# Kernel tuning notes

Measured on AMD Instinct MI355X. Metric: run time of the kernel, lower is better.

Reference implementation:

```python
import jax, jax.numpy as jnp
import numpy as np

T, B, D = 2048, 1, 1024
N_HEAD, D_HEAD, D_FF = 16, 64, 4096
LN_EPS = 1e-5


def layer_norm(x, g, b):
    m = jnp.mean(x, axis=-1, keepdims=True)
    v = jnp.mean(jnp.square(x - m), axis=-1, keepdims=True)
    return (x - m) * jax.lax.rsqrt(v + LN_EPS) * g + b


def rel_shift(x):
    # x: (qlen, klen, bsz, n_head) -> Transformer-XL relative shift
    q, k, b, h = x.shape
    zp = jnp.zeros((q, 1, b, h), dtype=x.dtype)
    x = jnp.concatenate([zp, x], axis=1)            # (q, k+1, b, h)
    x = x.reshape(k + 1, q, b, h)[1:].reshape(q, k, b, h)
    return x


def setup_inputs() -> dict:
    key = jax.random.key(0)
    ks = jax.random.split(key, 12)
    s = lambda fan: 1.0 / np.sqrt(fan)
    inp = {
        "input": jax.random.normal(ks[0], (T, B, D), jnp.float32),
        "pos": jax.random.normal(ks[1], (T, 1, D), jnp.float32),
        "r_w_bias": jax.random.normal(ks[2], (N_HEAD, D_HEAD), jnp.float32) * 0.02,
        "r_r_bias": jax.random.normal(ks[3], (N_HEAD, D_HEAD), jnp.float32) * 0.02,
        # causal mask: True = masked (future positions)
        "mask": jnp.triu(jnp.ones((T, T), dtype=bool), k=1),
        "ln1_g": jnp.ones((D,), jnp.float32),
        "ln1_b": jnp.zeros((D,), jnp.float32),
        "qkv_w": jax.random.normal(ks[4], (D, 3 * D), jnp.float32) * s(D),
        "r_w": jax.random.normal(ks[5], (D, D), jnp.float32) * s(D),
        "o_w": jax.random.normal(ks[6], (D, D), jnp.float32) * s(D),
        "ln2_g": jnp.ones((D,), jnp.float32),
        "ln2_b": jnp.zeros((D,), jnp.float32),
        "ff_w1": jax.random.normal(ks[7], (D, D_FF), jnp.float32) * s(D),
        "ff_b1": jnp.zeros((D_FF,), jnp.float32),
        "ff_w2": jax.random.normal(ks[8], (D_FF, D), jnp.float32) * s(D_FF),
        "ff_b2": jnp.zeros((D,), jnp.float32),
    }
    return inp


def reference(input, pos, r_w_bias, r_r_bias, mask, ln1_g, ln1_b, qkv_w, r_w,
              o_w, ln2_g, ln2_b, ff_w1, ff_b1, ff_w2, ff_b2):
    scale = 1.0 / np.sqrt(D_HEAD)
    # preprocess_attn: layernorm
    q_in = layer_norm(input, ln1_g, ln1_b)                      # (T,B,D)
    w_heads = jnp.einsum('tbd,de->tbe', q_in, qkv_w)            # (T,B,3D)
    w_q, w_k, w_v = jnp.split(w_heads, 3, axis=-1)
    w_q = w_q.reshape(T, B, N_HEAD, D_HEAD)
    w_k = w_k.reshape(T, B, N_HEAD, D_HEAD)
    w_v = w_v.reshape(T, B, N_HEAD, D_HEAD)
    r_k = (pos[:, 0] @ r_w).reshape(T, N_HEAD, D_HEAD)          # (T,h,dh)

    AC = jnp.einsum('ibnd,jbnd->ijbn', w_q + r_w_bias, w_k)     # (T,T,B,h)
    BD = rel_shift(jnp.einsum('ibnd,jnd->ijbn', w_q + r_r_bias, r_k))
    score = (AC + BD) * scale
    score = jnp.where(mask[:, :, None, None], jnp.finfo(score.dtype).min, score)
    probs = jax.nn.softmax(score, axis=1)                       # coverage
    attn_vec = jnp.einsum('ijbn,jbnd->ibnd', probs, w_v).reshape(T, B, D)
    attn_out = jnp.einsum('tbd,de->tbe', attn_vec, o_w)
    # postprocess_attn: (dropout=identity) + residual
    x = input + attn_out
    # FFN block: layernorm > linear-relu-linear > residual
    y = layer_norm(x, ln2_g, ln2_b)
    y = jax.nn.relu(jnp.einsum('tbd,df->tbf', y, ff_w1) + ff_b1)
    y = jnp.einsum('tbf,fd->tbd', y, ff_w2) + ff_b2
    x = x + y
    return x, probs
```

## Files before the change

### kernel.cpp

```cpp
#include <hip/hip_runtime.h>
#include <hip/hip_bf16.h>
#include <stdint.h>

using bf16 = __hip_bfloat16;
using short8 = __attribute__((ext_vector_type(8))) short;
using f32x4 = __attribute__((ext_vector_type(4))) float;

#define T_SEQ 2048
#define DMODEL 1024
#define NHEAD 16
#define DHEAD 64
#define DFF 4096

struct __align__(8) bf16x4 { bf16 x, y, z, w; };

__device__ __forceinline__ void async_cp16(const bf16* g, bf16* l) {
  __builtin_amdgcn_global_load_lds(
      (const __attribute__((address_space(1))) uint32_t*)g,
      (__attribute__((address_space(3))) uint32_t*)l, 16, 0, 0);
}

__global__ __launch_bounds__(256) void transpose_all(
    const float* __restrict__ s0, bf16* __restrict__ d0,
    const float* __restrict__ s1, bf16* __restrict__ d1,
    const float* __restrict__ s2, bf16* __restrict__ d2,
    const float* __restrict__ s3, bf16* __restrict__ d3,
    const float* __restrict__ s4, bf16* __restrict__ d4,
    const float* __restrict__ s5, bf16* __restrict__ d5) {
  __shared__ float tile[32][33];
  int b = blockIdx.x;
  int tx = threadIdx.x, ty = threadIdx.y;
  if (b >= 13312) {
    int idx = (b - 13312) * 256 + ty * 32 + tx;
    float4 v = ((const float4*)s5)[idx];
    bf16x4 o{__float2bfloat16(v.x), __float2bfloat16(v.y),
             __float2bfloat16(v.z), __float2bfloat16(v.w)};
    ((bf16x4*)d5)[idx] = o;
    return;
  }
  const float* src; bf16* dst; int R, C, t;
  if (b < 3072)      { src = s0; dst = d0; R = 1024; C = 3072; t = b; }
  else if (b < 4096) { src = s1; dst = d1; R = 1024; C = 1024; t = b - 3072; }
  else if (b < 5120) { src = s2; dst = d2; R = 1024; C = 1024; t = b - 4096; }
  else if (b < 9216) { src = s3; dst = d3; R = 1024; C = 4096; t = b - 5120; }
  else               { src = s4; dst = d4; R = 4096; C = 1024; t = b - 9216; }
  int tcols = C >> 5;
  int bx = (t % tcols) * 32;
  int by = (t / tcols) * 32;
#pragma unroll
  for (int r = 0; r < 32; r += 8)
    tile[ty + r][tx] = src[(long)(by + ty + r) * C + bx + tx];
  __syncthreads();
#pragma unroll
  for (int r = 0; r < 32; r += 8)
    dst[(long)(bx + ty + r) * R + by + tx] = __float2bfloat16(tile[tx][ty + r]);
}

__global__ __launch_bounds__(256) void ln_cvt(const float* __restrict__ x,
                                              const float* __restrict__ g,
                                              const float* __restrict__ b,
                                              bf16* __restrict__ out) {
  int row = blockIdx.x;
  int tid = threadIdx.x;
  float4 v = ((const float4*)(x + (long)row * DMODEL))[tid];
  float s = v.x + v.y + v.z + v.w;
  float s2 = v.x * v.x + v.y * v.y + v.z * v.z + v.w * v.w;
#pragma unroll
  for (int off = 32; off > 0; off >>= 1) {
    s += __shfl_down(s, off);
    s2 += __shfl_down(s2, off);
  }
  __shared__ float ss[4], ss2[4];
  int wave = tid >> 6, lane = tid & 63;
  if (lane == 0) { ss[wave] = s; ss2[wave] = s2; }
  __syncthreads();
  s = ss[0] + ss[1] + ss[2] + ss[3];
  s2 = ss2[0] + ss2[1] + ss2[2] + ss2[3];
  float mean = s * (1.0f / DMODEL);
  float var = s2 * (1.0f / DMODEL) - mean * mean;
  float rstd = rsqrtf(var + 1e-5f);
  float4 gg = ((const float4*)g)[tid];
  float4 bb = ((const float4*)b)[tid];
  bf16x4 o{__float2bfloat16((v.x - mean) * rstd * gg.x + bb.x),
           __float2bfloat16((v.y - mean) * rstd * gg.y + bb.y),
           __float2bfloat16((v.z - mean) * rstd * gg.z + bb.z),
           __float2bfloat16((v.w - mean) * rstd * gg.w + bb.w)};
  ((bf16x4*)(out + (long)row * DMODEL))[tid] = o;
}

__global__ __launch_bounds__(256) void ff2_init(const float* __restrict__ xws,
                                                const float* __restrict__ b2,
                                                float* __restrict__ out) {
  int idx = blockIdx.x * 256 + threadIdx.x;
  float4 x = ((const float4*)xws)[idx];
  float4 b = ((const float4*)b2)[idx & 255];
  float4 o{x.x + b.x, x.y + b.y, x.z + b.z, x.w + b.w};
  ((float4*)out)[idx] = o;
}

template <int BM, int BN, class Epi>
__global__ __launch_bounds__(256) void gemm_bt(const bf16* __restrict__ A,
                                               const bf16* __restrict__ Bt,
                                               int M, int N, int K,
                                               long aZstride, long bZstride, Epi epi) {
  constexpr int BK = 32;
  constexpr int MT = BM / 32;
  constexpr int NT = BN / 32;
  __shared__ bf16 As[BM * BK];
  __shared__ bf16 Bs[BN * BK];

  const int bm = blockIdx.y, bn = blockIdx.x, z = blockIdx.z;
  const bf16* Ab = A + (long)z * aZstride;
  const bf16* Bb = Bt + (long)z * bZstride;

  const int tid = threadIdx.x;
  const int lane = tid & 63;
  const int wave = tid >> 6;
  const int wr = wave >> 1;
  const int wc = wave & 1;
  const int kBeg = epi.kmin(bm, bn, z);
  const int kEnd = epi.kmax(bm, bn, z, K);

  const f32x4 zero4 = {0.f, 0.f, 0.f, 0.f};
  f32x4 acc[MT][NT];
#pragma unroll
  for (int mt = 0; mt < MT; ++mt)
#pragma unroll
    for (int nt = 0; nt < NT; ++nt) acc[mt][nt] = zero4;

  const int sr = tid >> 2;
  const int sc = (tid & 3) * 8;
  const bf16* aG0 = Ab + (long)(bm * BM + sr) * K + kBeg + sc;
  const bf16* aG1 = Ab + (long)(bm * BM + 64 + sr) * K + kBeg + sc;
  bf16* aL0 = As + tid * 8;
  bf16* aL1 = As + 2048 + tid * 8;
  const bf16* bG0 = Bb + (long)(bn * BN + sr) * K + kBeg + sc;
  bf16* bL0 = Bs + tid * 8;
  const bf16* bG1 = Bb + (long)(bn * BN + 64 + sr) * K + kBeg + sc;
  bf16* bL1 = Bs + 2048 + tid * 8;

  const int aRow = wr * (BM / 2) + (lane & 15);
  const int bRow = wc * (BN / 2) + (lane & 15);
  const int kq = (lane >> 4) * 8;

  for (int k0 = kBeg; k0 < kEnd; k0 += BK) {
    __syncthreads();
    async_cp16(aG0, aL0);
    if constexpr (BM == 128) async_cp16(aG1, aL1);
    async_cp16(bG0, bL0);
    if constexpr (BN == 128) async_cp16(bG1, bL1);
    aG0 += BK; bG0 += BK;
    if constexpr (BM == 128) aG1 += BK;
    if constexpr (BN == 128) bG1 += BK;
    __syncthreads();
    short8 af[MT], bfr[NT];
#pragma unroll
    for (int mt = 0; mt < MT; ++mt)
      af[mt] = *(const short8*)(As + (aRow + mt * 16) * BK + kq);
#pragma unroll
    for (int nt = 0; nt < NT; ++nt)
      bfr[nt] = *(const short8*)(Bs + (bRow + nt * 16) * BK + kq);
#pragma unroll
    for (int mt = 0; mt < MT; ++mt)
#pragma unroll
      for (int nt = 0; nt < NT; ++nt)
        acc[mt][nt] = __builtin_amdgcn_mfma_f32_16x16x32_bf16(af[mt], bfr[nt],
                                                              acc[mt][nt], 0, 0, 0);
  }

  const int rBase = (lane >> 4) * 4;
  const int cOff = lane & 15;
#pragma unroll
  for (int mt = 0; mt < MT; ++mt) {
#pragma unroll
    for (int nt = 0; nt < NT; ++nt) {
      int row = bm * BM + wr * (BM / 2) + mt * 16 + rBase;
      int col = bn * BN + wc * (BN / 2) + nt * 16 + cOff;
      f32x4 v = acc[mt][nt];
#pragma unroll
      for (int r = 0; r < 4; ++r) epi.store(z, row + r, col, v[r]);
    }
  }
}

struct EpiQKV {
  bf16 *Qh, *Kb, *Vt;
  __device__ int kmin(int, int, int) const { return 0; }
  __device__ int kmax(int, int, int, int K) const { return K; }
  __device__ void store(int, int row, int col, float v) const {
    int n = (col >> 6) & 15, d = col & 63;
    long hoff = ((long)n * T_SEQ + row) * DHEAD + d;
    if (col < DMODEL) {
      Qh[hoff] = __float2bfloat16(v);
    } else if (col < 2 * DMODEL) {
      Kb[hoff] = __float2bfloat16(v);
    } else {
      Vt[((long)n * DHEAD + d) * T_SEQ + row] = __float2bfloat16(v);
    }
  }
};

struct EpiRk {
  bf16* Rk;
  __device__ int kmin(int, int, int) const { return 0; }
  __device__ int kmax(int, int, int, int K) const { return K; }
  __device__ void store(int, int row, int col, float v) const {
    int n = col >> 6, d = col & 63;
    Rk[((long)n * T_SEQ + row) * DHEAD + d] = __float2bfloat16(v);
  }
};

struct EpiPV {
  bf16* av;
  __device__ int kmin(int, int, int) const { return 0; }
  __device__ int kmax(int bm, int, int, int K) const {
    int kl = ((bm >> 1) + 1) * 128;
    return kl < K ? kl : K;
  }
  __device__ void store(int z, int row, int col, float v) const {
    av[(long)row * DMODEL + z * DHEAD + col] = __float2bfloat16(v);
  }
};

struct EpiO {
  float* xws;
  const float* inp;
  __device__ int kmin(int, int, int) const { return 0; }
  __device__ int kmax(int, int, int, int K) const { return K; }
  __device__ void store(int, int row, int col, float v) const {
    long idx = (long)row * DMODEL + col;
    xws[idx] = v + inp[idx];
  }
};

struct EpiFF1 {
  bf16* h;
  const float* b1;
  __device__ int kmin(int, int, int) const { return 0; }
  __device__ int kmax(int, int, int, int K) const { return K; }
  __device__ void store(int, int row, int col, float v) const {
    h[(long)row * DFF + col] = __float2bfloat16(fmaxf(v + b1[col], 0.f));
  }
};

struct EpiFF2 {
  float* out;
  __device__ int kmin(int, int, int z) const { return z * 1024; }
  __device__ int kmax(int, int, int z, int K) const {
    int e = z * 1024 + 1024;
    return e < K ? e : K;
  }
  __device__ void store(int, int row, int col, float v) const {
    unsafeAtomicAdd(&out[(long)row * DMODEL + col], v);
  }
};

__global__ __launch_bounds__(256) void bias_k(const bf16* __restrict__ Kb,
                                              const bf16* __restrict__ Rk,
                                              const float* __restrict__ rwb,
                                              const float* __restrict__ rrb,
                                              float* __restrict__ acB,
                                              float* __restrict__ rrbR) {
  int idx = blockIdx.x * 256 + threadIdx.x;
  int n = idx >> 11;
  const short8* kp = (const short8*)(Kb + (long)idx * DHEAD);
  const short8* rp = (const short8*)(Rk + (long)idx * DHEAD);
  float s1 = 0.f, s2 = 0.f;
#pragma unroll
  for (int q8 = 0; q8 < 8; ++q8) {
    short8 kv = kp[q8], rv = rp[q8];
#pragma unroll
    for (int e = 0; e < 8; ++e) {
      float w1 = rwb[n * DHEAD + q8 * 8 + e];
      float w2 = rrb[n * DHEAD + q8 * 8 + e];
      s1 += w1 * __bfloat162float(((const bf16*)&kv)[e]);
      s2 += w2 * __bfloat162float(((const bf16*)&rv)[e]);
    }
  }
  acB[idx] = s1;
  rrbR[idx] = s2;
}

__global__ __launch_bounds__(256) void score_k(const bf16* __restrict__ Qh,
                                               const bf16* __restrict__ Kb,
                                               const bf16* __restrict__ Rk,
                                               const float* __restrict__ acB,
                                               const float* __restrict__ rrbR,
                                               bf16* __restrict__ score) {
  const int bn = blockIdx.x, bm = blockIdx.y, z = blockIdx.z;
  if (bn > bm) return;
  __shared__ char smem[70656];
  bf16* Qs  = (bf16*)smem;
  bf16* Ks  = (bf16*)(smem + 16384);
  bf16* Bnd = (bf16*)(smem + 32768);

  const int tid = threadIdx.x;
  const int lane = tid & 63, wave = tid >> 6;
  const int wr = wave >> 1, wc = wave & 1;
  const int kq = (lane >> 4) * 8;
  const int l15 = lane & 15;
  const int base = 128 * (bn - bm) + T_SEQ - 1 - 128;

  const bf16* Qg = Qh + ((long)z * T_SEQ + bm * 128) * DHEAD;
  const bf16* Kg = Kb + ((long)z * T_SEQ + bn * 128) * DHEAD;
  const bf16* Rg = Rk + (long)z * T_SEQ * DHEAD;

#pragma unroll
  for (int it = 0; it < 4; ++it) {
    int s = it * 256 + tid;
    int kh = s >> 9, r = (s >> 2) & 127, c = (s & 3) * 8;
    async_cp16(Qg + (long)r * DHEAD + kh * 32 + c, Qs + s * 8);
    async_cp16(Kg + (long)r * DHEAD + kh * 32 + c, Ks + s * 8);
  }
#pragma unroll
  for (int it = 0; it < 8; ++it) {
    int s = it * 256 + tid;
    int kh = s >> 10, u = (s >> 2) & 255, c = (s & 3) * 8;
    int g = base + u;
    g = g < 0 ? 0 : (g > T_SEQ - 1 ? T_SEQ - 1 : g);
    async_cp16(Rg + (long)g * DHEAD + kh * 32 + c, Bnd + s * 8);
  }

  const f32x4 zero4 = {0.f, 0.f, 0.f, 0.f};
  f32x4 accA[4][4], accW[4][8];
#pragma unroll
  for (int mt = 0; mt < 4; ++mt) {
#pragma unroll
    for (int nt = 0; nt < 4; ++nt) accA[mt][nt] = zero4;
#pragma unroll
    for (int ut = 0; ut < 8; ++ut) accW[mt][ut] = zero4;
  }

  __syncthreads();
#pragma unroll
  for (int kh = 0; kh < 2; ++kh) {
    short8 qa[4], kf[4], wf[8];
#pragma unroll
    for (int mt = 0; mt < 4; ++mt)
      qa[mt] = *(const short8*)(Qs + kh * 4096 + (wr * 64 + mt * 16 + l15) * 32 + kq);
#pragma unroll
    for (int nt = 0; nt < 4; ++nt)
      kf[nt] = *(const short8*)(Ks + kh * 4096 + (wc * 64 + nt * 16 + l15) * 32 + kq);
#pragma unroll
    for (int ut = 0; ut < 8; ++ut)
      wf[ut] = *(const short8*)(Bnd + kh * 8192 + (wc * 128 + ut * 16 + l15) * 32 + kq);
#pragma unroll
    for (int mt = 0; mt < 4; ++mt) {
#pragma unroll
      for (int nt = 0; nt < 4; ++nt)
        accA[mt][nt] = __builtin_amdgcn_mfma_f32_16x16x32_bf16(qa[mt], kf[nt], accA[mt][nt], 0, 0, 0);
#pragma unroll
      for (int ut = 0; ut < 8; ++ut)
        accW[mt][ut] = __builtin_amdgcn_mfma_f32_16x16x32_bf16(qa[mt], wf[ut], accW[mt][ut], 0, 0, 0);
    }
  }

  float wbias[8];
#pragma unroll
  for (int ut = 0; ut < 8; ++ut) {
    int u = wc * 128 + ut * 16 + l15;
    int g = base + u;
    g = g < 0 ? 0 : (g > T_SEQ - 1 ? T_SEQ - 1 : g);
    wbias[ut] = rrbR[(long)z * T_SEQ + g];
  }
  float abias[4];
#pragma unroll
  for (int nt = 0; nt < 4; ++nt)
    abias[nt] = acB[(long)z * T_SEQ + bn * 128 + wc * 64 + nt * 16 + l15];

  __syncthreads();

  bf16* Wl = (bf16*)smem + wr * (64 * 276);
  const int quad4 = (lane >> 4) * 4;
  const int umin = wr ? 1 : 65;
  const int umax = wr ? 191 : 255;
#pragma unroll
  for (int mt = 0; mt < 4; ++mt) {
#pragma unroll
    for (int ut = 0; ut < 8; ++ut) {
      int ub = wc * 128 + ut * 16;
      if (ub + 15 < umin || ub > umax) continue;
      int lr = mt * 16 + quad4;
      int u = ub + l15;
#pragma unroll
      for (int reg = 0; reg < 4; ++reg)
        Wl[(lr + reg) * 276 + u] = __float2bfloat16(accW[mt][ut][reg] + wbias[ut]);
    }
  }
  __syncthreads();

  bf16* srow = score + (long)z * T_SEQ * T_SEQ;
#pragma unroll
  for (int mt = 0; mt < 4; ++mt) {
#pragma unroll
    for (int nt = 0; nt < 4; ++nt) {
      int lr = mt * 16 + quad4;
      int c = wc * 64 + nt * 16 + l15;
#pragma unroll
      for (int reg = 0; reg < 4; ++reg) {
        int rl = lr + reg;
        int r = wr * 64 + rl;
        int u = c - r + 128;
        float v = accA[mt][nt][reg] + abias[nt] +
                  __bfloat162float(Wl[rl * 276 + u]);
        srow[(long)(bm * 128 + r) * T_SEQ + bn * 128 + c] = __float2bfloat16(v);
      }
    }
  }
}

__global__ __launch_bounds__(1024) void softmax_k(const bf16* __restrict__ S,
                                                  float* __restrict__ probs,
                                                  bf16* __restrict__ pb) {
  constexpr int HS = T_SEQ + 8;
  __shared__ bf16 pl[NHEAD * HS];
  __shared__ float rinv_s[NHEAD];
  const int i = blockIdx.x;
  const int tid = threadIdx.x;
  const int h = tid >> 6, lane = tid & 63;
  const float scale = 0.125f;
  const int nch = (i >> 9) + 1;

  const bf16* row = S + (long)h * T_SEQ * T_SEQ + (long)i * T_SEQ;

  short8 v[4];
  float m = -1e30f;
#pragma unroll
  for (int c = 0; c < 4; ++c) {
    if (c < nch) {
      int j0 = c * 512 + lane * 8;
      v[c] = *(const short8*)(row + j0);
#pragma unroll
      for (int e = 0; e < 8; ++e) {
        float s = (j0 + e <= i) ? __bfloat162float(((const bf16*)&v[c])[e]) * scale : -1e30f;
        m = fmaxf(m, s);
      }
    }
  }
#pragma unroll
  for (int off = 1; off < 64; off <<= 1) m = fmaxf(m, __shfl_xor(m, off));

  float l = 0.f;
#pragma unroll
  for (int c = 0; c < 4; ++c) {
    if (c < nch) {
      int j0 = c * 512 + lane * 8;
      short8 o;
#pragma unroll
      for (int e = 0; e < 8; ++e) {
        float p = 0.f;
        if (j0 + e <= i) {
          p = __expf(__bfloat162float(((const bf16*)&v[c])[e]) * scale - m);
          l += p;
        }
        ((bf16*)&o)[e] = __float2bfloat16(p);
      }
      *(short8*)(pl + h * HS + j0) = o;
    }
  }
#pragma unroll
  for (int off = 1; off < 64; off <<= 1) l += __shfl_xor(l, off);
  if (lane == 0) rinv_s[h] = 1.f / l;
  __syncthreads();

  float* prow = probs + (long)i * T_SEQ * NHEAD;
  const int n0 = (tid & 3) * 4;
  const float rv0 = rinv_s[n0 + 0], rv1 = rinv_s[n0 + 1];
  const float rv2 = rinv_s[n0 + 2], rv3 = rinv_s[n0 + 3];
#pragma unroll
  for (int it = 0; it < 8; ++it) {
    int o = it * 1024 + tid;
    int j = o >> 2;
    float4 f = {0.f, 0.f, 0.f, 0.f};
    if (j <= i) {
      f.x = __bfloat162float(pl[(n0 + 0) * HS + j]) * rv0;
      f.y = __bfloat162float(pl[(n0 + 1) * HS + j]) * rv1;
      f.z = __bfloat162float(pl[(n0 + 2) * HS + j]) * rv2;
      f.w = __bfloat162float(pl[(n0 + 3) * HS + j]) * rv3;
    }
    ((float4*)prow)[o] = f;
  }

  const int kround = ((i >> 7) + 1) << 7;
  bf16* prow_b = pb + (long)h * T_SEQ * T_SEQ + (long)i * T_SEQ;
  const float rinv = rinv_s[h];
  for (int j0 = lane * 8; j0 < kround; j0 += 512) {
    short8 pv = *(const short8*)(pl + h * HS + j0);
    short8 o;
#pragma unroll
    for (int e = 0; e < 8; ++e)
      ((bf16*)&o)[e] = __float2bfloat16(__bfloat162float(((const bf16*)&pv)[e]) * rinv);
    *(short8*)(prow_b + j0) = o;
  }
}

extern "C" void kernel_launch(void* const* d_in, const int* in_sizes, int n_in,
                              void* d_out, int out_size, void* d_ws, size_t ws_size,
                              hipStream_t stream) {
  const float* input = (const float*)d_in[0];
  const float* pos   = (const float*)d_in[1];
  const float* rwb   = (const float*)d_in[2];
  const float* rrb   = (const float*)d_in[3];
  const float* ln1g  = (const float*)d_in[5];
  const float* ln1b  = (const float*)d_in[6];
  const float* qkvw  = (const float*)d_in[7];
  const float* rw    = (const float*)d_in[8];
  const float* ow    = (const float*)d_in[9];
  const float* ln2g  = (const float*)d_in[10];
  const float* ln2b  = (const float*)d_in[11];
  const float* ffw1  = (const float*)d_in[12];
  const float* ffb1  = (const float*)d_in[13];
  const float* ffw2  = (const float*)d_in[14];
  const float* ffb2  = (const float*)d_in[15];
  float* out = (float*)d_out;

  size_t off = 0;
  auto alloc = [&](size_t bytes) -> char* {
    char* p = (char*)d_ws + off;
    off += (bytes + 255) & ~(size_t)255;
    return p;
  };
  bf16* wqkvT = (bf16*)alloc(3072L * 1024 * 2);
  bf16* wrT   = (bf16*)alloc(1024L * 1024 * 2);
  bf16* woT   = (bf16*)alloc(1024L * 1024 * 2);
  bf16* wf1T  = (bf16*)alloc(4096L * 1024 * 2);
  bf16* wf2T  = (bf16*)alloc(1024L * 4096 * 2);
  bf16* qin   = (bf16*)alloc(2048L * 1024 * 2);
  bf16* posb  = (bf16*)alloc(2048L * 1024 * 2);
  bf16* Qh    = (bf16*)alloc(16L * 2048 * 64 * 2);
  bf16* Kb    = (bf16*)alloc(16L * 2048 * 64 * 2);
  bf16* Vt    = (bf16*)alloc(16L * 64 * 2048 * 2);
  bf16* Rk    = (bf16*)alloc(16L * 2048 * 64 * 2);
  float* acB  = (float*)alloc(16L * 2048 * 4);
  float* rrbR = (float*)alloc(16L * 2048 * 4);
  bf16* ACb   = (bf16*)alloc(16L * 2048 * 2048 * 2);
  bf16* pb    = (bf16*)alloc(16L * 2048 * 2048 * 2);
  bf16* av    = (bf16*)alloc(2048L * 1024 * 2);
  float* xws  = (float*)alloc(2048L * 1024 * 4);
  bf16* yb    = (bf16*)alloc(2048L * 1024 * 2);
  bf16* hb    = (bf16*)alloc(2048L * 4096 * 2);

  dim3 tb(32, 8);
  transpose_all<<<15360, tb, 0, stream>>>(qkvw, wqkvT, rw, wrT, ow, woT,
                                          ffw1, wf1T, ffw2, wf2T, pos, posb);
  ln_cvt<<<2048, 256, 0, stream>>>(input, ln1g, ln1b, qin);

  {
    EpiQKV e{Qh, Kb, Vt};
    gemm_bt<128, 128, EpiQKV><<<dim3(24, 16, 1), 256, 0, stream>>>(qin, wqkvT, 2048, 3072, 1024, 0, 0, e);
  }
  {
    EpiRk e{Rk};
    gemm_bt<64, 64, EpiRk><<<dim3(16, 32, 1), 256, 0, stream>>>(posb, wrT, 2048, 1024, 1024, 0, 0, e);
  }
  bias_k<<<128, 256, 0, stream>>>(Kb, Rk, rwb, rrb, acB, rrbR);
  score_k<<<dim3(16, 16, 16), 256, 0, stream>>>(Qh, Kb, Rk, acB, rrbR, ACb);
  softmax_k<<<2048, 1024, 0, stream>>>(ACb, out + 2048L * 1024, pb);
  {
    EpiPV e{av};
    gemm_bt<64, 64, EpiPV><<<dim3(1, 32, 16), 256, 0, stream>>>(pb, Vt, 2048, 64, 2048,
                                                                2048L * 2048, 64L * 2048, e);
  }
  {
    EpiO e{xws, input};
    gemm_bt<64, 64, EpiO><<<dim3(16, 32, 1), 256, 0, stream>>>(av, woT, 2048, 1024, 1024, 0, 0, e);
  }
  ff2_init<<<2048, 256, 0, stream>>>(xws, ffb2, out);
  ln_cvt<<<2048, 256, 0, stream>>>(xws, ln2g, ln2b, yb);
  {
    EpiFF1 e{hb, ffb1};
    gemm_bt<128, 128, EpiFF1><<<dim3(32, 16, 1), 256, 0, stream>>>(yb, wf1T, 2048, 4096, 1024, 0, 0, e);
  }
  {
    EpiFF2 e{out};
    gemm_bt<128, 64, EpiFF2><<<dim3(16, 16, 4), 256, 0, stream>>>(hb, wf2T, 2048, 1024, 4096, 0, 0, e);
  }
}
```

Baseline: 733.2 us.

## Double-buffer GEMM LDS tiles and use larger K-steps for small tiles

Converts the bf16 GEMM main loop to a double-buffered LDS pipeline: it prefetches the next K tile with async global-to-LDS loads while computing MFMAs on the current one, and needs only one barrier per iteration instead of two. It also templates BK, using 64 for the 64x64 and 128x64 GEMMs so fewer loop iterations and barriers are needed. The cost is twice the LDS per block, which may lower occupancy. The same barrier also guards the in-flight async loads, so correctness depends on those loads completing in time.

```diff
diff --git a/kernel.cpp b/kernel.cpp
--- a/kernel.cpp
+++ b/kernel.cpp
@@ -18,6 +18,22 @@
   __builtin_amdgcn_global_load_lds(
       (const __attribute__((address_space(1))) uint32_t*)g,
       (__attribute__((address_space(3))) uint32_t*)l, 16, 0, 0);
+}
+
+template <int ROWS, int BK>
+__device__ __forceinline__ void stage_tile(const bf16* __restrict__ g, int ldg,
+                                           bf16* l, int tid) {
+  constexpr int PAN = ROWS * 32;
+  constexpr int ROUNDS = ROWS * BK / 2048;
+#pragma unroll
+  for (int r = 0; r < ROUNDS; ++r) {
+    int off = (r * 256 + tid) * 8;
+    int kkp = off / PAN;
+    int rem = off % PAN;
+    int row = rem >> 5;
+    int col = kkp * 32 + (rem & 31);
+    async_cp16(g + (long)row * ldg + col, l + off);
+  }
 }
 
 __global__ __launch_bounds__(256) void transpose_all(
@@ -98,20 +114,20 @@
   ((float4*)out)[idx] = o;
 }
 
-template <int BM, int BN, class Epi>
+template <int BM, int BN, int BK, class Epi>
 __global__ __launch_bounds__(256) void gemm_bt(const bf16* __restrict__ A,
                                                const bf16* __restrict__ Bt,
                                                int M, int N, int K,
                                                long aZstride, long bZstride, Epi epi) {
-  constexpr int BK = 32;
   constexpr int MT = BM / 32;
   constexpr int NT = BN / 32;
-  __shared__ bf16 As[BM * BK];
-  __shared__ bf16 Bs[BN * BK];
+  constexpr int KK = BK / 32;
+  __shared__ bf16 As[2][BM * BK];
+  __shared__ bf16 Bs[2][BN * BK];
 
   const int bm = blockIdx.y, bn = blockIdx.x, z = blockIdx.z;
-  const bf16* Ab = A + (long)z * aZstride;
-  const bf16* Bb = Bt + (long)z * bZstride;
+  const bf16* Ab = A + (long)z * aZstride + (long)bm * BM * K;
+  const bf16* Bb = Bt + (long)z * bZstride + (long)bn * BN * K;
 
   const int tid = threadIdx.x;
   const int lane = tid & 63;
@@ -128,44 +144,41 @@
 #pragma unroll
     for (int nt = 0; nt < NT; ++nt) acc[mt][nt] = zero4;
 
-  const int sr = tid >> 2;
-  const int sc = (tid & 3) * 8;
-  const bf16* aG0 = Ab + (long)(bm * BM + sr) * K + kBeg + sc;
-  const bf16* aG1 = Ab + (long)(bm * BM + 64 + sr) * K + kBeg + sc;
-  bf16* aL0 = As + tid * 8;
-  bf16* aL1 = As + 2048 + tid * 8;
-  const bf16* bG0 = Bb + (long)(bn * BN + sr) * K + kBeg + sc;
-  bf16* bL0 = Bs + tid * 8;
-  const bf16* bG1 = Bb + (long)(bn * BN + 64 + sr) * K + kBeg + sc;
-  bf16* bL1 = Bs + 2048 + tid * 8;
-
   const int aRow = wr * (BM / 2) + (lane & 15);
   const int bRow = wc * (BN / 2) + (lane & 15);
   const int kq = (lane >> 4) * 8;
 
+  stage_tile<BM, BK>(Ab + kBeg, K, As[0], tid);
+  stage_tile<BN, BK>(Bb + kBeg, K, Bs[0], tid);
+  __syncthreads();
+
+  int cur = 0;
   for (int k0 = kBeg; k0 < kEnd; k0 += BK) {
+    int kn = k0 + BK;
+    if (kn < kEnd) {
+      stage_tile<BM, BK>(Ab + kn, K, As[cur ^ 1], tid);
+      stage_tile<BN, BK>(Bb + kn, K, Bs[cur ^ 1], tid);
+    }
+    short8 af[KK][MT], bfr[KK][NT];
+#pragma unroll
+    for (int kk = 0; kk < KK; ++kk) {
+#pragma unroll
+      for (int mt = 0; mt < MT; ++mt)
+        af[kk][mt] = *(const short8*)(&As[cur][kk * (BM * 32) + (aRow + mt * 16) * 32 + kq]);
+#pragma unroll
+      for (int nt = 0; nt < NT; ++nt)
+        bfr[kk][nt] = *(const short8*)(&Bs[cur][kk * (BN * 32) + (bRow + nt * 16) * 32 + kq]);
+    }
+#pragma unroll
+    for (int kk = 0; kk < KK; ++kk)
+#pragma unroll
+      for (int mt = 0; mt < MT; ++mt)
+#pragma unroll
+        for (int nt = 0; nt < NT; ++nt)
+          acc[mt][nt] = __builtin_amdgcn_mfma_f32_16x16x32_bf16(af[kk][mt], bfr[kk][nt],
+                                                                acc[mt][nt], 0, 0, 0);
     __syncthreads();
-    async_cp16(aG0, aL0);
-    if constexpr (BM == 128) async_cp16(aG1, aL1);
-    async_cp16(bG0, bL0);
-    if constexpr (BN == 128) async_cp16(bG1, bL1);
-    aG0 += BK; bG0 += BK;
-    if constexpr (BM == 128) aG1 += BK;
-    if constexpr (BN == 128) bG1 += BK;
-    __syncthreads();
-    short8 af[MT], bfr[NT];
-#pragma unroll
-    for (int mt = 0; mt < MT; ++mt)
-      af[mt] = *(const short8*)(As + (aRow + mt * 16) * BK + kq);
-#pragma unroll
-    for (int nt = 0; nt < NT; ++nt)
-      bfr[nt] = *(const short8*)(Bs + (bRow + nt * 16) * BK + kq);
-#pragma unroll
-    for (int mt = 0; mt < MT; ++mt)
-#pragma unroll
-      for (int nt = 0; nt < NT; ++nt)
-        acc[mt][nt] = __builtin_amdgcn_mfma_f32_16x16x32_bf16(af[mt], bfr[nt],
-                                                              acc[mt][nt], 0, 0, 0);
+    cur ^= 1;
   }
 
   const int rBase = (lane >> 4) * 4;
@@ -547,32 +560,32 @@
 
   {
     EpiQKV e{Qh, Kb, Vt};
-    gemm_bt<128, 128, EpiQKV><<<dim3(24, 16, 1), 256, 0, stream>>>(qin, wqkvT, 2048, 3072, 1024, 0, 0, e);
+    gemm_bt<128, 128, 32, EpiQKV><<<dim3(24, 16, 1), 256, 0, stream>>>(qin, wqkvT, 2048, 3072, 1024, 0, 0, e);
   }
   {
     EpiRk e{Rk};
-    gemm_bt<64, 64, EpiRk><<<dim3(16, 32, 1), 256, 0, stream>>>(posb, wrT, 2048, 1024, 1024, 0, 0, e);
+    gemm_bt<64, 64, 64, EpiRk><<<dim3(16, 32, 1), 256, 0, stream>>>(posb, wrT, 2048, 1024, 1024, 0, 0, e);
   }
   bias_k<<<128, 256, 0, stream>>>(Kb, Rk, rwb, rrb, acB, rrbR);
   score_k<<<dim3(16, 16, 16), 256, 0, stream>>>(Qh, Kb, Rk, acB, rrbR, ACb);
   softmax_k<<<2048, 1024, 0, stream>>>(ACb, out + 2048L * 1024, pb);
   {
     EpiPV e{av};
-    gemm_bt<64, 64, EpiPV><<<dim3(1, 32, 16), 256, 0, stream>>>(pb, Vt, 2048, 64, 2048,
-                                                                2048L * 2048, 64L * 2048, e);
+    gemm_bt<64, 64, 64, EpiPV><<<dim3(1, 32, 16), 256, 0, stream>>>(pb, Vt, 2048, 64, 2048,
+                                                                    2048L * 2048, 64L * 2048, e);
   }
   {
     EpiO e{xws, input};
-    gemm_bt<64, 64, EpiO><<<dim3(16, 32, 1), 256, 0, stream>>>(av, woT, 2048, 1024, 1024, 0, 0, e);
+    gemm_bt<64, 64, 64, EpiO><<<dim3(16, 32, 1), 256, 0, stream>>>(av, woT, 2048, 1024, 1024, 0, 0, e);
   }
   ff2_init<<<2048, 256, 0, stream>>>(xws, ffb2, out);
   ln_cvt<<<2048, 256, 0, stream>>>(xws, ln2g, ln2b, yb);
   {
     EpiFF1 e{hb, ffb1};
-    gemm_bt<128, 128, EpiFF1><<<dim3(32, 16, 1), 256, 0, stream>>>(yb, wf1T, 2048, 4096, 1024, 0, 0, e);
+    gemm_bt<128, 128, 32, EpiFF1><<<dim3(32, 16, 1), 256, 0, stream>>>(yb, wf1T, 2048, 4096, 1024, 0, 0, e);
   }
   {
     EpiFF2 e{out};
-    gemm_bt<128, 64, EpiFF2><<<dim3(16, 16, 4), 256, 0, stream>>>(hb, wf2T, 2048, 1024, 4096, 0, 0, e);
-  }
-}
+    gemm_bt<128, 64, 64, EpiFF2><<<dim3(16, 16, 4), 256, 0, stream>>>(hb, wf2T, 2048, 1024, 4096, 0, 0, e);
+  }
+}
```

Measured after the change: 724.9 us. Within noise of the previous version (-1.1%).
